# Performance work log

Measured on AMD Instinct MI355X. Metric: run time of the kernel, lower is better.

## Reference

```python
import jax, jax.numpy as jnp
import numpy as np

B, S, I, H, C = 256, 128, 512, 1024, 10
VOCAB = S  # nn.Embedding(seq_length, input_dim)


def _lstm_dir(embeds_tbi, W, b):
    """Run an LSTM over time. embeds_tbi: [S,B,I]; W: [4H, I+H] stacked (g,i,f,o); b: [4H]."""
    h0 = jnp.zeros((B, H), jnp.float32)
    c0 = jnp.zeros((B, H), jnp.float32)

    def step(carry, x_t):
        c, h = carry
        xh = jnp.concatenate([x_t, h], axis=1)          # [B, I+H]
        z = xh @ W.T + b                                 # [B, 4H]
        g, i, f, o = jnp.split(z, 4, axis=1)
        g = jnp.tanh(g)
        i = jax.nn.sigmoid(i)
        f = jax.nn.sigmoid(f)
        o = jax.nn.sigmoid(o)
        new_c = g * i + c * f
        new_h = jnp.tanh(new_c) * o
        return (new_c, new_h), None

    (c_T, h_T), _ = jax.lax.scan(step, (c0, h0), embeds_tbi)
    return h_T


def setup_inputs() -> dict:
    key = jax.random.key(0)
    ks = jax.random.split(key, 8)
    x = jax.random.randint(ks[0], (B, S), 0, VOCAB)
    embed = jax.random.normal(ks[1], (VOCAB, I), jnp.float32) * 0.5
    scale = 1.0 / np.sqrt(I + H)
    fwd_W = jax.random.normal(ks[2], (4 * H, I + H), jnp.float32) * scale  # stacked g,i,f,o
    fwd_b = jax.random.normal(ks[3], (4 * H,), jnp.float32) * 0.02
    bwd_W = jax.random.normal(ks[4], (4 * H, I + H), jnp.float32) * scale
    bwd_b = jax.random.normal(ks[5], (4 * H,), jnp.float32) * 0.02
    p_w = jax.random.normal(ks[6], (C, 2 * H), jnp.float32) * (1.0 / np.sqrt(2 * H))
    p_b = jax.random.normal(ks[7], (C,), jnp.float32) * 0.02
    return {"x": x, "embed": embed, "fwd_W": fwd_W, "fwd_b": fwd_b,
            "bwd_W": bwd_W, "bwd_b": bwd_b, "p_w": p_w, "p_b": p_b}


def reference(x, embed, fwd_W, fwd_b, bwd_W, bwd_b, p_w, p_b):
    embeds = embed[x]                       # [B,S,I]
    emb_t = jnp.transpose(embeds, (1, 0, 2))  # [S,B,I]
    h_fwd = _lstm_dir(emb_t, fwd_W, fwd_b)
    h_bwd = _lstm_dir(emb_t[::-1], bwd_W, bwd_b)
    h_comb = jnp.concatenate([h_fwd, h_bwd], axis=1)  # [B,2H]
    return jax.nn.log_softmax(h_comb @ p_w.T + p_b, axis=1)
```

## Files before the change

### kernel.cpp

```cpp
#include <hip/hip_runtime.h>
#include <hip/hip_bf16.h>
#include <math.h>

#define B 256
#define S 128
#define I_DIM 512
#define H 1024
#define C 10
#define WROW 1536

#define LDS_H 131072

typedef float f32x4 __attribute__((ext_vector_type(4), may_alias));
typedef __bf16 bf16x8 __attribute__((ext_vector_type(8), may_alias));
typedef unsigned int u32x4 __attribute__((ext_vector_type(4), may_alias));
typedef unsigned long long u64;
typedef unsigned long long __attribute__((may_alias)) u64a;

__device__ __forceinline__ unsigned short f2bf(float f) {
    union { float f; unsigned u; } a; a.f = f;
    return (unsigned short)((a.u + 0x7fffu + ((a.u >> 16) & 1u)) >> 16);
}
__device__ __forceinline__ float sigf(float v) { return 1.0f / (1.0f + __expf(-v)); }
__device__ __forceinline__ float tanh_fast(float v) { return 1.0f - 2.0f / (1.0f + __expf(2.0f * v)); }

__global__ void wf_build(const float* __restrict__ fwd_W,
                         const float* __restrict__ bwd_W,
                         __hip_bfloat16* __restrict__ wF) {
    int gid = blockIdx.x * 256 + threadIdx.x;
    int lane = gid & 63, kk = (gid >> 6) & 31, nsub = (gid >> 11) & 255, d = gid >> 19;
    int n_gl = nsub * 16 + (lane & 15);
    int j = n_gl >> 2, g = n_gl & 3;
    int k = kk * 32 + (lane >> 4) * 8;
    const float* W = d ? bwd_W : fwd_W;
    const float* src = W + (size_t)(g * 1024 + j) * WROW + I_DIM + k;
    ushort4 lo = make_ushort4(f2bf(src[0]), f2bf(src[1]), f2bf(src[2]), f2bf(src[3]));
    ushort4 hi = make_ushort4(f2bf(src[4]), f2bf(src[5]), f2bf(src[6]), f2bf(src[7]));
    ushort4* dst = (ushort4*)(wF + (size_t)gid * 8);
    dst[0] = lo; dst[1] = hi;
}

__global__ void projp_kernel(const float* __restrict__ embed,
                             const float* __restrict__ fwd_W,
                             const float* __restrict__ fwd_b,
                             const float* __restrict__ bwd_W,
                             const float* __restrict__ bwd_b,
                             float* __restrict__ projP) {
    __shared__ float wrows[16][520];
    int d  = blockIdx.x >> 8;
    int nc = blockIdx.x & 255;
    int n0 = nc * 16;
    const float* W    = d ? bwd_W : fwd_W;
    const float* bias = d ? bwd_b : fwd_b;
    int tid = threadIdx.x;
    for (int i = tid; i < 16 * 128; i += 256) {
        int r = i >> 7, kc = i & 127;
        *(f32x4*)&wrows[r][kc * 4] = *(const f32x4*)(W + (size_t)(n0 + r) * WROW + kc * 4);
    }
    __syncthreads();
    const int r = tid & 15, vg = tid >> 4;
    const float* eb = embed + (size_t)(vg * 8) * I_DIM;
    f32x4 acc[8] = {};
    for (int kc = 0; kc < 128; kc++) {
        f32x4 w = *(const f32x4*)&wrows[r][kc * 4];
#pragma unroll
        for (int vi = 0; vi < 8; vi++) {
            f32x4 e = *(const f32x4*)(eb + (size_t)vi * I_DIM + kc * 4);
            acc[vi] += w * e;
        }
    }
    const int n = n0 + r, g = n >> 10, j = n & 1023;
    const float bv = bias[n];
    float* outp = projP + ((size_t)d * 1024 + j) * 128 * 4 + g;
#pragma unroll
    for (int vi = 0; vi < 8; vi++) {
        float s = acc[vi][0] + acc[vi][1] + acc[vi][2] + acc[vi][3] + bv;
        outp[(vg * 8 + vi) * 4] = s;
    }
}

__global__ __launch_bounds__(512, 1) void step_kernel(
        const int* __restrict__ x,
        const __hip_bfloat16* __restrict__ wF,
        const float* __restrict__ projP,
        __hip_bfloat16* __restrict__ hbuf,
        float* __restrict__ cws,
        int t) {
    extern __shared__ char smem[];
    const int bid = blockIdx.x;
    const int xcd = bid & 7, idx = bid >> 3;
    const int slot = idx >> 2, bt = idx & 3;
    const int grp = slot * 8 + xcd;
    const int d = grp >> 5, jt = grp & 31;
    const int tid = threadIdx.x, wid = tid >> 6, lane = tid & 63;
    const int l15 = lane & 15, l4 = lane >> 4;
    const int b0 = bt * 64;
    const size_t dBH = (size_t)d * B * H;

    const __hip_bfloat16* wp = wF + (size_t)(d * 256 + jt * 8 + wid) * 16384;

    bf16x8 Ap[8];
    if (t > 0) {
#pragma unroll
        for (int p = 0; p < 8; p++)
            Ap[p] = *(const bf16x8*)(wp + p * 512 + lane * 8);
    }
    const int tt = d ? (S - 1 - t) : t;
    int vv[4];
#pragma unroll
    for (int bs = 0; bs < 4; bs++)
        vv[bs] = x[(b0 + bs * 16 + l15) * S + tt];

    float* cp = cws + ((size_t)bid * 512 + tid) * 4;
    f32x4 cv = {0.f, 0.f, 0.f, 0.f};
    if (t > 0) cv = *(const f32x4*)cp;

    if (t > 0) {
        const __hip_bfloat16* hr = hbuf + (size_t)(t & 1) * 2 * B * H + dBH + (size_t)b0 * H;
#pragma unroll
        for (int i = 0; i < 16; i++) {
            int flat = i * 512 + tid;
            int row = flat >> 7, c16 = flat & 127;
            u32x4 v = *(const u32x4*)(hr + (size_t)row * H + c16 * 8);
            *(u32x4*)(smem + row * 2048 + ((c16 * 16) ^ ((row & 7) << 4))) = v;
        }
    }

    const int j = jt * 32 + wid * 4 + l4;
    const f32x4* pp = (const f32x4*)projP + ((size_t)d * 1024 + j) * 128;
    f32x4 pj[4];
#pragma unroll
    for (int bs = 0; bs < 4; bs++) pj[bs] = pp[vv[bs]];

    f32x4 acc[4] = {};
    if (t > 0) {
        __syncthreads();
        int brow[4], bswz[4];
#pragma unroll
        for (int bs = 0; bs < 4; bs++) {
            int row = bs * 16 + l15;
            brow[bs] = row * 2048;
            bswz[bs] = (row & 7) << 4;
        }
        bf16x8 Bcur[4];
#pragma unroll
        for (int bs = 0; bs < 4; bs++)
            Bcur[bs] = *(const bf16x8*)(smem + brow[bs] + ((l4 * 16) ^ bswz[bs]));
#pragma unroll
        for (int kk = 0; kk < 32; kk++) {
            bf16x8 A = Ap[kk & 7];
            if (kk < 24)
                Ap[kk & 7] = *(const bf16x8*)(wp + (kk + 8) * 512 + lane * 8);
            bf16x8 B0 = Bcur[0], B1 = Bcur[1], B2 = Bcur[2], B3 = Bcur[3];
            if (kk < 31) {
                int koff = (kk + 1) * 64 + l4 * 16;
#pragma unroll
                for (int bs = 0; bs < 4; bs++)
                    Bcur[bs] = *(const bf16x8*)(smem + brow[bs] + (koff ^ bswz[bs]));
            }
            acc[0] = __builtin_amdgcn_mfma_f32_16x16x32_bf16(A, B0, acc[0], 0, 0, 0);
            acc[1] = __builtin_amdgcn_mfma_f32_16x16x32_bf16(A, B1, acc[1], 0, 0, 0);
            acc[2] = __builtin_amdgcn_mfma_f32_16x16x32_bf16(A, B2, acc[2], 0, 0, 0);
            acc[3] = __builtin_amdgcn_mfma_f32_16x16x32_bf16(A, B3, acc[3], 0, 0, 0);
        }
    }

    float hnv[4];
#pragma unroll
    for (int bs = 0; bs < 4; bs++) {
        float zg = acc[bs][0] + pj[bs][0];
        float zi = acc[bs][1] + pj[bs][1];
        float zf = acc[bs][2] + pj[bs][2];
        float zo = acc[bs][3] + pj[bs][3];
        float gg = tanh_fast(zg);
        float ii = sigf(zi);
        float ff = sigf(zf);
        float oo = sigf(zo);
        float cn = gg * ii + cv[bs] * ff;
        cv[bs] = cn;
        hnv[bs] = tanh_fast(cn) * oo;
    }
    *(f32x4*)cp = cv;

    unsigned plo = (unsigned)f2bf(hnv[0]) | ((unsigned)f2bf(hnv[1]) << 16);
    unsigned phi = (unsigned)f2bf(hnv[2]) | ((unsigned)f2bf(hnv[3]) << 16);
    unsigned short o4[4];
#pragma unroll
    for (int p = 0; p < 4; p++) {
        int src = p * 16 + l15;
        unsigned vlo = __shfl(plo, src);
        unsigned vhi = __shfl(phi, src);
        unsigned sel = (l4 < 2) ? vlo : vhi;
        o4[p] = (l4 & 1) ? (unsigned short)(sel >> 16) : (unsigned short)(sel & 0xffffu);
    }
    u64 hv = (u64)o4[0] | ((u64)o4[1] << 16) | ((u64)o4[2] << 32) | ((u64)o4[3] << 48);
    __hip_bfloat16* hw = hbuf + (size_t)((t + 1) & 1) * 2 * B * H + dBH
                         + (size_t)(b0 + lane) * H + jt * 32 + wid * 4;
    *(u64a*)hw = hv;
}

__global__ void head_kernel(const __hip_bfloat16* __restrict__ hbuf,
                            const float* __restrict__ p_w,
                            const float* __restrict__ p_b,
                            float* __restrict__ out) {
    int b = blockIdx.x;
    int lane = threadIdx.x;
    float part[C];
#pragma unroll
    for (int cc = 0; cc < C; cc++) part[cc] = 0.0f;
    for (int jj = lane; jj < 2 * H; jj += 64) {
        float hv = (jj < H)
            ? __bfloat162float(hbuf[(size_t)b * H + jj])
            : __bfloat162float(hbuf[(size_t)B * H + (size_t)b * H + jj - H]);
#pragma unroll
        for (int cc = 0; cc < C; cc++) part[cc] += hv * p_w[cc * 2 * H + jj];
    }
#pragma unroll
    for (int cc = 0; cc < C; cc++) {
        float v = part[cc];
        for (int off = 32; off; off >>= 1) v += __shfl_down(v, off);
        part[cc] = v;
    }
    if (lane == 0) {
        float lg[C];
        float m = -1e30f;
        for (int cc = 0; cc < C; cc++) {
            lg[cc] = part[cc] + p_b[cc];
            m = fmaxf(m, lg[cc]);
        }
        float s = 0.0f;
        for (int cc = 0; cc < C; cc++) s += expf(lg[cc] - m);
        float lse = logf(s) + m;
        for (int cc = 0; cc < C; cc++) out[b * C + cc] = lg[cc] - lse;
    }
}

extern "C" void kernel_launch(void* const* d_in, const int* in_sizes, int n_in,
                              void* d_out, int out_size, void* d_ws, size_t ws_size,
                              hipStream_t stream) {
    const int*   x     = (const int*)d_in[0];
    const float* embed = (const float*)d_in[1];
    const float* fwd_W = (const float*)d_in[2];
    const float* fwd_b = (const float*)d_in[3];
    const float* bwd_W = (const float*)d_in[4];
    const float* bwd_b = (const float*)d_in[5];
    const float* p_w   = (const float*)d_in[6];
    const float* p_b   = (const float*)d_in[7];
    float* outp = (float*)d_out;

    char* ws = (char*)d_ws;
    __hip_bfloat16* wF = (__hip_bfloat16*)ws;  ws += (size_t)2 * 256 * 16384 * 2;
    float* projP = (float*)ws;                 ws += (size_t)2 * 1024 * 128 * 4 * 4;
    __hip_bfloat16* hbuf = (__hip_bfloat16*)ws; ws += (size_t)2 * 2 * B * H * 2;
    float* cws = (float*)ws;                   ws += (size_t)256 * 512 * 4 * 4;

    hipLaunchKernelGGL(wf_build, dim3(4096), dim3(256), 0, stream, fwd_W, bwd_W, wF);
    hipLaunchKernelGGL(projp_kernel, dim3(512), dim3(256), 0, stream,
                       embed, fwd_W, fwd_b, bwd_W, bwd_b, projP);

    hipFuncSetAttribute((const void*)step_kernel,
                        hipFuncAttributeMaxDynamicSharedMemorySize, LDS_H);

    for (int t = 0; t < S; t++)
        hipLaunchKernelGGL(step_kernel, dim3(256), dim3(512), LDS_H, stream,
                           x, wF, projP, hbuf, cws, t);

    hipLaunchKernelGGL(head_kernel, dim3(B), dim3(64), 0, stream,
                       hbuf, p_w, p_b, outp);
}
```

Measured before the change: 1.554 ms.

## Replace per-step launches with a persistent cooperative kernel using flag-based sync

```diff
diff --git a/kernel.cpp b/kernel.cpp
--- a/kernel.cpp
+++ b/kernel.cpp
@@ -15,7 +15,6 @@
 typedef __bf16 bf16x8 __attribute__((ext_vector_type(8), may_alias));
 typedef unsigned int u32x4 __attribute__((ext_vector_type(4), may_alias));
 typedef unsigned long long u64;
-typedef unsigned long long __attribute__((may_alias)) u64a;
 
 __device__ __forceinline__ unsigned short f2bf(float f) {
     union { float f; unsigned u; } a; a.f = f;
@@ -46,7 +45,7 @@
                              const float* __restrict__ bwd_W,
                              const float* __restrict__ bwd_b,
                              float* __restrict__ projP) {
-    __shared__ float wrows[16][520];
+    __shared__ float wrows[16][516];
     int d  = blockIdx.x >> 8;
     int nc = blockIdx.x & 255;
     int n0 = nc * 16;
@@ -79,124 +78,172 @@
     }
 }
 
-__global__ __launch_bounds__(512, 1) void step_kernel(
+__device__ __forceinline__ void stage8(const __hip_bfloat16* hr, int r0, int cc,
+                                       char* smem, int ibase) {
+    const void* p0 = (const void*)(hr + (size_t)((ibase + 0) * 4 + r0) * H + cc * 8);
+    const void* p1 = (const void*)(hr + (size_t)((ibase + 1) * 4 + r0) * H + cc * 8);
+    const void* p2 = (const void*)(hr + (size_t)((ibase + 2) * 4 + r0) * H + cc * 8);
+    const void* p3 = (const void*)(hr + (size_t)((ibase + 3) * 4 + r0) * H + cc * 8);
+    const void* p4 = (const void*)(hr + (size_t)((ibase + 4) * 4 + r0) * H + cc * 8);
+    const void* p5 = (const void*)(hr + (size_t)((ibase + 5) * 4 + r0) * H + cc * 8);
+    const void* p6 = (const void*)(hr + (size_t)((ibase + 6) * 4 + r0) * H + cc * 8);
+    const void* p7 = (const void*)(hr + (size_t)((ibase + 7) * 4 + r0) * H + cc * 8);
+    u32x4 s0, s1, s2, s3, s4, s5, s6, s7;
+    asm volatile(
+        "global_load_dwordx4 %0, %8, off sc0 sc1\n\t"
+        "global_load_dwordx4 %1, %9, off sc0 sc1\n\t"
+        "global_load_dwordx4 %2, %10, off sc0 sc1\n\t"
+        "global_load_dwordx4 %3, %11, off sc0 sc1\n\t"
+        "global_load_dwordx4 %4, %12, off sc0 sc1\n\t"
+        "global_load_dwordx4 %5, %13, off sc0 sc1\n\t"
+        "global_load_dwordx4 %6, %14, off sc0 sc1\n\t"
+        "global_load_dwordx4 %7, %15, off sc0 sc1\n\t"
+        "s_waitcnt vmcnt(0)"
+        : "=&v"(s0), "=&v"(s1), "=&v"(s2), "=&v"(s3),
+          "=&v"(s4), "=&v"(s5), "=&v"(s6), "=&v"(s7)
+        : "v"(p0), "v"(p1), "v"(p2), "v"(p3), "v"(p4), "v"(p5), "v"(p6), "v"(p7)
+        : "memory");
+    int row;
+    row = (ibase + 0) * 4 + r0; *(u32x4*)(smem + row * 2048 + ((cc * 16) ^ ((row & 7) << 4))) = s0;
+    row = (ibase + 1) * 4 + r0; *(u32x4*)(smem + row * 2048 + ((cc * 16) ^ ((row & 7) << 4))) = s1;
+    row = (ibase + 2) * 4 + r0; *(u32x4*)(smem + row * 2048 + ((cc * 16) ^ ((row & 7) << 4))) = s2;
+    row = (ibase + 3) * 4 + r0; *(u32x4*)(smem + row * 2048 + ((cc * 16) ^ ((row & 7) << 4))) = s3;
+    row = (ibase + 4) * 4 + r0; *(u32x4*)(smem + row * 2048 + ((cc * 16) ^ ((row & 7) << 4))) = s4;
+    row = (ibase + 5) * 4 + r0; *(u32x4*)(smem + row * 2048 + ((cc * 16) ^ ((row & 7) << 4))) = s5;
+    row = (ibase + 6) * 4 + r0; *(u32x4*)(smem + row * 2048 + ((cc * 16) ^ ((row & 7) << 4))) = s6;
+    row = (ibase + 7) * 4 + r0; *(u32x4*)(smem + row * 2048 + ((cc * 16) ^ ((row & 7) << 4))) = s7;
+}
+
+__global__ __launch_bounds__(512, 2) void bilstm_persistent(
         const int* __restrict__ x,
         const __hip_bfloat16* __restrict__ wF,
         const float* __restrict__ projP,
         __hip_bfloat16* __restrict__ hbuf,
-        float* __restrict__ cws,
-        int t) {
+        unsigned* __restrict__ flags) {
     extern __shared__ char smem[];
     const int bid = blockIdx.x;
-    const int xcd = bid & 7, idx = bid >> 3;
-    const int slot = idx >> 2, bt = idx & 3;
-    const int grp = slot * 8 + xcd;
-    const int d = grp >> 5, jt = grp & 31;
+    const int xcd = bid & 7;
+    const int d = xcd >> 2, jtHi = xcd & 3;
+    const int idx = bid >> 3;
+    const int jtLo = idx >> 2, bt = idx & 3;
+    const int jt = jtHi * 8 + jtLo;
     const int tid = threadIdx.x, wid = tid >> 6, lane = tid & 63;
     const int l15 = lane & 15, l4 = lane >> 4;
     const int b0 = bt * 64;
     const size_t dBH = (size_t)d * B * H;
 
     const __hip_bfloat16* wp = wF + (size_t)(d * 256 + jt * 8 + wid) * 16384;
-
-    bf16x8 Ap[8];
-    if (t > 0) {
-#pragma unroll
-        for (int p = 0; p < 8; p++)
-            Ap[p] = *(const bf16x8*)(wp + p * 512 + lane * 8);
-    }
-    const int tt = d ? (S - 1 - t) : t;
-    int vv[4];
-#pragma unroll
-    for (int bs = 0; bs < 4; bs++)
-        vv[bs] = x[(b0 + bs * 16 + l15) * S + tt];
-
-    float* cp = cws + ((size_t)bid * 512 + tid) * 4;
-    f32x4 cv = {0.f, 0.f, 0.f, 0.f};
-    if (t > 0) cv = *(const f32x4*)cp;
-
-    if (t > 0) {
-        const __hip_bfloat16* hr = hbuf + (size_t)(t & 1) * 2 * B * H + dBH + (size_t)b0 * H;
-#pragma unroll
-        for (int i = 0; i < 16; i++) {
-            int flat = i * 512 + tid;
-            int row = flat >> 7, c16 = flat & 127;
-            u32x4 v = *(const u32x4*)(hr + (size_t)row * H + c16 * 8);
-            *(u32x4*)(smem + row * 2048 + ((c16 * 16) ^ ((row & 7) << 4))) = v;
-        }
-    }
-
     const int j = jt * 32 + wid * 4 + l4;
     const f32x4* pp = (const f32x4*)projP + ((size_t)d * 1024 + j) * 128;
-    f32x4 pj[4];
-#pragma unroll
-    for (int bs = 0; bs < 4; bs++) pj[bs] = pp[vv[bs]];
-
-    f32x4 acc[4] = {};
-    if (t > 0) {
+    const int r0 = tid >> 7;
+    const int cc = tid & 127;
+
+    int brow[4], bswz[4];
+#pragma unroll
+    for (int bs = 0; bs < 4; bs++) {
+        int row = bs * 16 + l15;
+        brow[bs] = row * 2048;
+        bswz[bs] = (row & 7) << 4;
+    }
+
+    float cst[4] = {0.f, 0.f, 0.f, 0.f};
+
+    for (int t = 0; t < S; t++) {
+        if (t > 0) {
+            if (tid == 0) {
+                const unsigned* p = flags + (size_t)((t - 1) * 8 + d * 4 + bt) * 16;
+                while (__hip_atomic_load(p, __ATOMIC_RELAXED, __HIP_MEMORY_SCOPE_AGENT) < 32u)
+                    __builtin_amdgcn_s_sleep(4);
+            }
+            __syncthreads();
+        }
+
+        bf16x8 Ap[8];
+        if (t > 0) {
+#pragma unroll
+            for (int p = 0; p < 8; p++)
+                Ap[p] = *(const bf16x8*)(wp + p * 512 + lane * 8);
+        }
+        const int tt = d ? (S - 1 - t) : t;
+        int vv[4];
+#pragma unroll
+        for (int bs = 0; bs < 4; bs++)
+            vv[bs] = x[(b0 + bs * 16 + l15) * S + tt];
+
+        if (t > 0) {
+            const __hip_bfloat16* hr = hbuf + (size_t)(t & 1) * 2 * B * H + dBH + (size_t)b0 * H;
+            stage8(hr, r0, cc, smem, 0);
+            stage8(hr, r0, cc, smem, 8);
+        }
+
+        f32x4 pj[4];
+#pragma unroll
+        for (int bs = 0; bs < 4; bs++) pj[bs] = pp[vv[bs]];
+
+        f32x4 acc[4] = {};
+        if (t > 0) {
+            __syncthreads();
+            bf16x8 Bcur[4];
+#pragma unroll
+            for (int bs = 0; bs < 4; bs++)
+                Bcur[bs] = *(const bf16x8*)(smem + brow[bs] + ((l4 * 16) ^ bswz[bs]));
+#pragma unroll
+            for (int kk = 0; kk < 32; kk++) {
+                bf16x8 A = Ap[kk & 7];
+                if (kk < 24)
+                    Ap[kk & 7] = *(const bf16x8*)(wp + (kk + 8) * 512 + lane * 8);
+                bf16x8 B0 = Bcur[0], B1 = Bcur[1], B2 = Bcur[2], B3 = Bcur[3];
+                if (kk < 31) {
+                    int koff = (kk + 1) * 64 + l4 * 16;
+#pragma unroll
+                    for (int bs = 0; bs < 4; bs++)
+                        Bcur[bs] = *(const bf16x8*)(smem + brow[bs] + (koff ^ bswz[bs]));
+                }
+                acc[0] = __builtin_amdgcn_mfma_f32_16x16x32_bf16(A, B0, acc[0], 0, 0, 0);
+                acc[1] = __builtin_amdgcn_mfma_f32_16x16x32_bf16(A, B1, acc[1], 0, 0, 0);
+                acc[2] = __builtin_amdgcn_mfma_f32_16x16x32_bf16(A, B2, acc[2], 0, 0, 0);
+                acc[3] = __builtin_amdgcn_mfma_f32_16x16x32_bf16(A, B3, acc[3], 0, 0, 0);
+            }
+        }
+
+        float hnv[4];
+#pragma unroll
+        for (int bs = 0; bs < 4; bs++) {
+            float zg = acc[bs][0] + pj[bs][0];
+            float zi = acc[bs][1] + pj[bs][1];
+            float zf = acc[bs][2] + pj[bs][2];
+            float zo = acc[bs][3] + pj[bs][3];
+            float gg = tanh_fast(zg);
+            float ii = sigf(zi);
+            float ff = sigf(zf);
+            float oo = sigf(zo);
+            float cn = gg * ii + cst[bs] * ff;
+            cst[bs] = cn;
+            hnv[bs] = tanh_fast(cn) * oo;
+        }
+
+        unsigned plo = (unsigned)f2bf(hnv[0]) | ((unsigned)f2bf(hnv[1]) << 16);
+        unsigned phi = (unsigned)f2bf(hnv[2]) | ((unsigned)f2bf(hnv[3]) << 16);
+        unsigned short o4[4];
+#pragma unroll
+        for (int p = 0; p < 4; p++) {
+            int src = p * 16 + l15;
+            unsigned vlo = __shfl(plo, src);
+            unsigned vhi = __shfl(phi, src);
+            unsigned sel = (l4 < 2) ? vlo : vhi;
+            o4[p] = (l4 & 1) ? (unsigned short)(sel >> 16) : (unsigned short)(sel & 0xffffu);
+        }
+        u64 hv = (u64)o4[0] | ((u64)o4[1] << 16) | ((u64)o4[2] << 32) | ((u64)o4[3] << 48);
+        void* hw = (void*)(hbuf + (size_t)((t + 1) & 1) * 2 * B * H + dBH
+                           + (size_t)(b0 + lane) * H + jt * 32 + wid * 4);
+        asm volatile("global_store_dwordx2 %0, %1, off sc0 sc1"
+                     :: "v"(hw), "v"(hv) : "memory");
+
         __syncthreads();
-        int brow[4], bswz[4];
-#pragma unroll
-        for (int bs = 0; bs < 4; bs++) {
-            int row = bs * 16 + l15;
-            brow[bs] = row * 2048;
-            bswz[bs] = (row & 7) << 4;
-        }
-        bf16x8 Bcur[4];
-#pragma unroll
-        for (int bs = 0; bs < 4; bs++)
-            Bcur[bs] = *(const bf16x8*)(smem + brow[bs] + ((l4 * 16) ^ bswz[bs]));
-#pragma unroll
-        for (int kk = 0; kk < 32; kk++) {
-            bf16x8 A = Ap[kk & 7];
-            if (kk < 24)
-                Ap[kk & 7] = *(const bf16x8*)(wp + (kk + 8) * 512 + lane * 8);
-            bf16x8 B0 = Bcur[0], B1 = Bcur[1], B2 = Bcur[2], B3 = Bcur[3];
-            if (kk < 31) {
-                int koff = (kk + 1) * 64 + l4 * 16;
-#pragma unroll
-                for (int bs = 0; bs < 4; bs++)
-                    Bcur[bs] = *(const bf16x8*)(smem + brow[bs] + (koff ^ bswz[bs]));
-            }
-            acc[0] = __builtin_amdgcn_mfma_f32_16x16x32_bf16(A, B0, acc[0], 0, 0, 0);
-            acc[1] = __builtin_amdgcn_mfma_f32_16x16x32_bf16(A, B1, acc[1], 0, 0, 0);
-            acc[2] = __builtin_amdgcn_mfma_f32_16x16x32_bf16(A, B2, acc[2], 0, 0, 0);
-            acc[3] = __builtin_amdgcn_mfma_f32_16x16x32_bf16(A, B3, acc[3], 0, 0, 0);
-        }
-    }
-
-    float hnv[4];
-#pragma unroll
-    for (int bs = 0; bs < 4; bs++) {
-        float zg = acc[bs][0] + pj[bs][0];
-        float zi = acc[bs][1] + pj[bs][1];
-        float zf = acc[bs][2] + pj[bs][2];
-        float zo = acc[bs][3] + pj[bs][3];
-        float gg = tanh_fast(zg);
-        float ii = sigf(zi);
-        float ff = sigf(zf);
-        float oo = sigf(zo);
-        float cn = gg * ii + cv[bs] * ff;
-        cv[bs] = cn;
-        hnv[bs] = tanh_fast(cn) * oo;
-    }
-    *(f32x4*)cp = cv;
-
-    unsigned plo = (unsigned)f2bf(hnv[0]) | ((unsigned)f2bf(hnv[1]) << 16);
-    unsigned phi = (unsigned)f2bf(hnv[2]) | ((unsigned)f2bf(hnv[3]) << 16);
-    unsigned short o4[4];
-#pragma unroll
-    for (int p = 0; p < 4; p++) {
-        int src = p * 16 + l15;
-        unsigned vlo = __shfl(plo, src);
-        unsigned vhi = __shfl(phi, src);
-        unsigned sel = (l4 < 2) ? vlo : vhi;
-        o4[p] = (l4 & 1) ? (unsigned short)(sel >> 16) : (unsigned short)(sel & 0xffffu);
-    }
-    u64 hv = (u64)o4[0] | ((u64)o4[1] << 16) | ((u64)o4[2] << 32) | ((u64)o4[3] << 48);
-    __hip_bfloat16* hw = hbuf + (size_t)((t + 1) & 1) * 2 * B * H + dBH
-                         + (size_t)(b0 + lane) * H + jt * 32 + wid * 4;
-    *(u64a*)hw = hv;
+        if (tid == 0)
+            __hip_atomic_fetch_add(flags + (size_t)(t * 8 + d * 4 + bt) * 16, 1u,
+                                   __ATOMIC_RELAXED, __HIP_MEMORY_SCOPE_AGENT);
+    }
 }
 
 __global__ void head_kernel(const __hip_bfloat16* __restrict__ hbuf,
@@ -252,18 +299,19 @@
     __hip_bfloat16* wF = (__hip_bfloat16*)ws;  ws += (size_t)2 * 256 * 16384 * 2;
     float* projP = (float*)ws;                 ws += (size_t)2 * 1024 * 128 * 4 * 4;
     __hip_bfloat16* hbuf = (__hip_bfloat16*)ws; ws += (size_t)2 * 2 * B * H * 2;
-    float* cws = (float*)ws;                   ws += (size_t)256 * 512 * 4 * 4;
-
+    unsigned* flags = (unsigned*)ws;           ws += (size_t)S * 8 * 16 * 4;
+
+    hipMemsetAsync(flags, 0, (size_t)S * 8 * 16 * 4, stream);
     hipLaunchKernelGGL(wf_build, dim3(4096), dim3(256), 0, stream, fwd_W, bwd_W, wF);
     hipLaunchKernelGGL(projp_kernel, dim3(512), dim3(256), 0, stream,
                        embed, fwd_W, fwd_b, bwd_W, bwd_b, projP);
 
-    hipFuncSetAttribute((const void*)step_kernel,
+    hipFuncSetAttribute((const void*)bilstm_persistent,
                         hipFuncAttributeMaxDynamicSharedMemorySize, LDS_H);
 
-    for (int t = 0; t < S; t++)
-        hipLaunchKernelGGL(step_kernel, dim3(256), dim3(512), LDS_H, stream,
-                           x, wF, projP, hbuf, cws, t);
+    void* args[] = {(void*)&x, (void*)&wF, (void*)&projP, (void*)&hbuf, (void*)&flags};
+    hipLaunchCooperativeKernel((void*)bilstm_persistent, dim3(256), dim3(512),
+                               args, LDS_H, stream);
 
     hipLaunchKernelGGL(head_kernel, dim3(B), dim3(64), 0, stream,
                        hbuf, p_w, p_b, outp);
```

New measurement: 1.546 ms. About the same (-0.5%).

## Use MFMA for input projection and split h staging into two halves

Applied to the files above, without the earlier changes.

```diff
diff --git a/kernel.cpp b/kernel.cpp
--- a/kernel.cpp
+++ b/kernel.cpp
@@ -20,6 +20,10 @@
 __device__ __forceinline__ unsigned short f2bf(float f) {
     union { float f; unsigned u; } a; a.f = f;
     return (unsigned short)((a.u + 0x7fffu + ((a.u >> 16) & 1u)) >> 16);
+}
+__device__ __forceinline__ float bf2f(unsigned short b) {
+    union { unsigned u; float f; } a; a.u = ((unsigned)b) << 16;
+    return a.f;
 }
 __device__ __forceinline__ float sigf(float v) { return 1.0f / (1.0f + __expf(-v)); }
 __device__ __forceinline__ float tanh_fast(float v) { return 1.0f - 2.0f / (1.0f + __expf(2.0f * v)); }
@@ -40,42 +44,92 @@
     dst[0] = lo; dst[1] = hi;
 }
 
-__global__ void projp_kernel(const float* __restrict__ embed,
-                             const float* __restrict__ fwd_W,
-                             const float* __restrict__ fwd_b,
-                             const float* __restrict__ bwd_W,
-                             const float* __restrict__ bwd_b,
-                             float* __restrict__ projP) {
-    __shared__ float wrows[16][520];
-    int d  = blockIdx.x >> 8;
-    int nc = blockIdx.x & 255;
-    int n0 = nc * 16;
-    const float* W    = d ? bwd_W : fwd_W;
-    const float* bias = d ? bwd_b : fwd_b;
-    int tid = threadIdx.x;
-    for (int i = tid; i < 16 * 128; i += 256) {
-        int r = i >> 7, kc = i & 127;
-        *(f32x4*)&wrows[r][kc * 4] = *(const f32x4*)(W + (size_t)(n0 + r) * WROW + kc * 4);
+__global__ void wxf_build(const float* __restrict__ fwd_W,
+                          const float* __restrict__ bwd_W,
+                          __hip_bfloat16* __restrict__ wxF) {
+    int gid = blockIdx.x * 256 + threadIdx.x;
+    int lane = gid & 63, kk = (gid >> 6) & 15, nsub = (gid >> 10) & 255, d = gid >> 18;
+    int n_gl = nsub * 16 + (lane & 15);
+    int j = n_gl >> 2, g = n_gl & 3;
+    int k = kk * 32 + (lane >> 4) * 8;
+    const float* W = d ? bwd_W : fwd_W;
+    const float* src = W + (size_t)(g * 1024 + j) * WROW + k;
+    ushort4 lo = make_ushort4(f2bf(src[0]), f2bf(src[1]), f2bf(src[2]), f2bf(src[3]));
+    ushort4 hi = make_ushort4(f2bf(src[4]), f2bf(src[5]), f2bf(src[6]), f2bf(src[7]));
+    ushort4* dst = (ushort4*)(wxF + (size_t)gid * 8);
+    dst[0] = lo; dst[1] = hi;
+}
+
+__global__ void ehl_build(const float* __restrict__ embed,
+                          unsigned short* __restrict__ ehl) {
+    int idx = blockIdx.x * 256 + threadIdx.x;
+    float e = embed[idx];
+    unsigned short hb = f2bf(e);
+    unsigned short lb = f2bf(e - bf2f(hb));
+    ehl[idx] = hb;
+    ehl[65536 + idx] = lb;
+}
+
+__global__ __launch_bounds__(256) void projp_mfma(
+        const __hip_bfloat16* __restrict__ wxF,
+        const unsigned short* __restrict__ ehl,
+        const float* __restrict__ fwd_b,
+        const float* __restrict__ bwd_b,
+        float* __restrict__ projP) {
+    extern __shared__ char sm[];
+    const int bid = blockIdx.x;
+    const int d = bid >> 7, jt = (bid >> 2) & 31, vb = bid & 3;
+    const int tid = threadIdx.x, w = tid >> 6, lane = tid & 63;
+    const int l15 = lane & 15, l4 = lane >> 4;
+    const int v0 = vb * 32;
+
+    for (int i = 0; i < 16; i++) {
+        int chunk = i * 256 + tid;
+        int row = chunk >> 6, c16 = chunk & 63;
+        int p = row >> 5, vs = v0 + (row & 31);
+        u32x4 vd = *(const u32x4*)(ehl + ((size_t)p * 128 + vs) * 512 + c16 * 8);
+        *(u32x4*)(sm + row * 1024 + ((c16 * 16) ^ ((row & 7) << 4))) = vd;
     }
     __syncthreads();
-    const int r = tid & 15, vg = tid >> 4;
-    const float* eb = embed + (size_t)(vg * 8) * I_DIM;
-    f32x4 acc[8] = {};
-    for (int kc = 0; kc < 128; kc++) {
-        f32x4 w = *(const f32x4*)&wrows[r][kc * 4];
-#pragma unroll
-        for (int vi = 0; vi < 8; vi++) {
-            f32x4 e = *(const f32x4*)(eb + (size_t)vi * I_DIM + kc * 4);
-            acc[vi] += w * e;
-        }
-    }
-    const int n = n0 + r, g = n >> 10, j = n & 1023;
-    const float bv = bias[n];
-    float* outp = projP + ((size_t)d * 1024 + j) * 128 * 4 + g;
-#pragma unroll
-    for (int vi = 0; vi < 8; vi++) {
-        float s = acc[vi][0] + acc[vi][1] + acc[vi][2] + acc[vi][3] + bv;
-        outp[(vg * 8 + vi) * 4] = s;
+
+    const __hip_bfloat16* ap0 = wxF + ((size_t)((d * 256 + jt * 8 + w * 2 + 0) * 16)) * 512;
+    const __hip_bfloat16* ap1 = wxF + ((size_t)((d * 256 + jt * 8 + w * 2 + 1) * 16)) * 512;
+    int hrow[2], hswz[2], lrow[2], lswz[2];
+#pragma unroll
+    for (int vt = 0; vt < 2; vt++) {
+        int hr = vt * 16 + l15, lr = hr + 32;
+        hrow[vt] = hr * 1024; hswz[vt] = (hr & 7) << 4;
+        lrow[vt] = lr * 1024; lswz[vt] = (lr & 7) << 4;
+    }
+    f32x4 acc[2][2] = {};
+#pragma unroll
+    for (int kk = 0; kk < 16; kk++) {
+        bf16x8 A0 = *(const bf16x8*)(ap0 + kk * 512 + lane * 8);
+        bf16x8 A1 = *(const bf16x8*)(ap1 + kk * 512 + lane * 8);
+        int ko = kk * 64 + l4 * 16;
+        bf16x8 Bh0 = *(const bf16x8*)(sm + hrow[0] + (ko ^ hswz[0]));
+        bf16x8 Bh1 = *(const bf16x8*)(sm + hrow[1] + (ko ^ hswz[1]));
+        bf16x8 Bl0 = *(const bf16x8*)(sm + lrow[0] + (ko ^ lswz[0]));
+        bf16x8 Bl1 = *(const bf16x8*)(sm + lrow[1] + (ko ^ lswz[1]));
+        acc[0][0] = __builtin_amdgcn_mfma_f32_16x16x32_bf16(A0, Bh0, acc[0][0], 0, 0, 0);
+        acc[0][0] = __builtin_amdgcn_mfma_f32_16x16x32_bf16(A0, Bl0, acc[0][0], 0, 0, 0);
+        acc[0][1] = __builtin_amdgcn_mfma_f32_16x16x32_bf16(A0, Bh1, acc[0][1], 0, 0, 0);
+        acc[0][1] = __builtin_amdgcn_mfma_f32_16x16x32_bf16(A0, Bl1, acc[0][1], 0, 0, 0);
+        acc[1][0] = __builtin_amdgcn_mfma_f32_16x16x32_bf16(A1, Bh0, acc[1][0], 0, 0, 0);
+        acc[1][0] = __builtin_amdgcn_mfma_f32_16x16x32_bf16(A1, Bl0, acc[1][0], 0, 0, 0);
+        acc[1][1] = __builtin_amdgcn_mfma_f32_16x16x32_bf16(A1, Bh1, acc[1][1], 0, 0, 0);
+        acc[1][1] = __builtin_amdgcn_mfma_f32_16x16x32_bf16(A1, Bl1, acc[1][1], 0, 0, 0);
+    }
+    const float* bp = d ? bwd_b : fwd_b;
+#pragma unroll
+    for (int nt = 0; nt < 2; nt++) {
+        int j = jt * 32 + w * 8 + nt * 4 + l4;
+        f32x4 bv = { bp[j], bp[1024 + j], bp[2048 + j], bp[3072 + j] };
+#pragma unroll
+        for (int vt = 0; vt < 2; vt++) {
+            int v = v0 + vt * 16 + l15;
+            *(f32x4*)(projP + ((size_t)(d * 1024 + j) * 128 + v) * 4) = acc[nt][vt] + bv;
+        }
     }
 }
 
@@ -88,10 +142,7 @@
         int t) {
     extern __shared__ char smem[];
     const int bid = blockIdx.x;
-    const int xcd = bid & 7, idx = bid >> 3;
-    const int slot = idx >> 2, bt = idx & 3;
-    const int grp = slot * 8 + xcd;
-    const int d = grp >> 5, jt = grp & 31;
+    const int d = bid >> 7, bt = (bid >> 5) & 3, jt = bid & 31;
     const int tid = threadIdx.x, wid = tid >> 6, lane = tid & 63;
     const int l15 = lane & 15, l4 = lane >> 4;
     const int b0 = bt * 64;
@@ -111,30 +162,39 @@
     for (int bs = 0; bs < 4; bs++)
         vv[bs] = x[(b0 + bs * 16 + l15) * S + tt];
 
+    u32x4 sb1[8], sb2[8];
+    int srow[8], sc16[8];
+    if (t > 0) {
+        const __hip_bfloat16* hr = hbuf + (size_t)(t & 1) * 2 * B * H + dBH + (size_t)b0 * H;
+#pragma unroll
+        for (int i = 0; i < 8; i++) {
+            int flat = i * 512 + tid;
+            srow[i] = flat >> 6;
+            sc16[i] = flat & 63;
+            sb1[i] = *(const u32x4*)(hr + (size_t)srow[i] * H + sc16[i] * 8);
+        }
+#pragma unroll
+        for (int i = 0; i < 8; i++)
+            sb2[i] = *(const u32x4*)(hr + (size_t)srow[i] * H + (sc16[i] + 64) * 8);
+    }
+
+    const int j = jt * 32 + wid * 4 + l4;
+    const f32x4* pp = (const f32x4*)projP + ((size_t)d * 1024 + j) * 128;
+    f32x4 pj[4];
+#pragma unroll
+    for (int bs = 0; bs < 4; bs++) pj[bs] = pp[vv[bs]];
+
     float* cp = cws + ((size_t)bid * 512 + tid) * 4;
     f32x4 cv = {0.f, 0.f, 0.f, 0.f};
     if (t > 0) cv = *(const f32x4*)cp;
 
-    if (t > 0) {
-        const __hip_bfloat16* hr = hbuf + (size_t)(t & 1) * 2 * B * H + dBH + (size_t)b0 * H;
-#pragma unroll
-        for (int i = 0; i < 16; i++) {
-            int flat = i * 512 + tid;
-            int row = flat >> 7, c16 = flat & 127;
-            u32x4 v = *(const u32x4*)(hr + (size_t)row * H + c16 * 8);
-            *(u32x4*)(smem + row * 2048 + ((c16 * 16) ^ ((row & 7) << 4))) = v;
-        }
-    }
-
-    const int j = jt * 32 + wid * 4 + l4;
-    const f32x4* pp = (const f32x4*)projP + ((size_t)d * 1024 + j) * 128;
-    f32x4 pj[4];
-#pragma unroll
-    for (int bs = 0; bs < 4; bs++) pj[bs] = pp[vv[bs]];
-
     f32x4 acc[4] = {};
     if (t > 0) {
+#pragma unroll
+        for (int i = 0; i < 8; i++)
+            *(u32x4*)(smem + srow[i] * 2048 + ((sc16[i] * 16) ^ ((srow[i] & 7) << 4))) = sb1[i];
         __syncthreads();
+
         int brow[4], bswz[4];
 #pragma unroll
         for (int bs = 0; bs < 4; bs++) {
@@ -142,22 +202,37 @@
             brow[bs] = row * 2048;
             bswz[bs] = (row & 7) << 4;
         }
-        bf16x8 Bcur[4];
-#pragma unroll
-        for (int bs = 0; bs < 4; bs++)
-            Bcur[bs] = *(const bf16x8*)(smem + brow[bs] + ((l4 * 16) ^ bswz[bs]));
-#pragma unroll
-        for (int kk = 0; kk < 32; kk++) {
+
+#pragma unroll
+        for (int kk = 0; kk < 16; kk++) {
+            bf16x8 A = Ap[kk & 7];
+            Ap[kk & 7] = *(const bf16x8*)(wp + (kk + 8) * 512 + lane * 8);
+            int koff = kk * 64 + l4 * 16;
+            bf16x8 B0 = *(const bf16x8*)(smem + brow[0] + (koff ^ bswz[0]));
+            bf16x8 B1 = *(const bf16x8*)(smem + brow[1] + (koff ^ bswz[1]));
+            bf16x8 B2 = *(const bf16x8*)(smem + brow[2] + (koff ^ bswz[2]));
+            bf16x8 B3 = *(const bf16x8*)(smem + brow[3] + (koff ^ bswz[3]));
+            acc[0] = __builtin_amdgcn_mfma_f32_16x16x32_bf16(A, B0, acc[0], 0, 0, 0);
+            acc[1] = __builtin_amdgcn_mfma_f32_16x16x32_bf16(A, B1, acc[1], 0, 0, 0);
+            acc[2] = __builtin_amdgcn_mfma_f32_16x16x32_bf16(A, B2, acc[2], 0, 0, 0);
+            acc[3] = __builtin_amdgcn_mfma_f32_16x16x32_bf16(A, B3, acc[3], 0, 0, 0);
+        }
+
+#pragma unroll
+        for (int i = 0; i < 8; i++)
+            *(u32x4*)(smem + srow[i] * 2048 + (((sc16[i] + 64) * 16) ^ ((srow[i] & 7) << 4))) = sb2[i];
+        __syncthreads();
+
+#pragma unroll
+        for (int kk = 16; kk < 32; kk++) {
             bf16x8 A = Ap[kk & 7];
             if (kk < 24)
                 Ap[kk & 7] = *(const bf16x8*)(wp + (kk + 8) * 512 + lane * 8);
-            bf16x8 B0 = Bcur[0], B1 = Bcur[1], B2 = Bcur[2], B3 = Bcur[3];
-            if (kk < 31) {
-                int koff = (kk + 1) * 64 + l4 * 16;
-#pragma unroll
-                for (int bs = 0; bs < 4; bs++)
-                    Bcur[bs] = *(const bf16x8*)(smem + brow[bs] + (koff ^ bswz[bs]));
-            }
+            int koff = kk * 64 + l4 * 16;
+            bf16x8 B0 = *(const bf16x8*)(smem + brow[0] + (koff ^ bswz[0]));
+            bf16x8 B1 = *(const bf16x8*)(smem + brow[1] + (koff ^ bswz[1]));
+            bf16x8 B2 = *(const bf16x8*)(smem + brow[2] + (koff ^ bswz[2]));
+            bf16x8 B3 = *(const bf16x8*)(smem + brow[3] + (koff ^ bswz[3]));
             acc[0] = __builtin_amdgcn_mfma_f32_16x16x32_bf16(A, B0, acc[0], 0, 0, 0);
             acc[1] = __builtin_amdgcn_mfma_f32_16x16x32_bf16(A, B1, acc[1], 0, 0, 0);
             acc[2] = __builtin_amdgcn_mfma_f32_16x16x32_bf16(A, B2, acc[2], 0, 0, 0);
@@ -249,18 +324,24 @@
     float* outp = (float*)d_out;
 
     char* ws = (char*)d_ws;
-    __hip_bfloat16* wF = (__hip_bfloat16*)ws;  ws += (size_t)2 * 256 * 16384 * 2;
-    float* projP = (float*)ws;                 ws += (size_t)2 * 1024 * 128 * 4 * 4;
+    __hip_bfloat16* wF  = (__hip_bfloat16*)ws;  ws += (size_t)2 * 256 * 16384 * 2;
+    __hip_bfloat16* wxF = (__hip_bfloat16*)ws;
+    float* cws = (float*)ws;                    ws += (size_t)2 * 256 * 8192 * 2;
+    unsigned short* ehl = (unsigned short*)ws;  ws += (size_t)2 * 128 * 512 * 2;
+    float* projP = (float*)ws;                  ws += (size_t)2 * 1024 * 128 * 4 * 4;
     __hip_bfloat16* hbuf = (__hip_bfloat16*)ws; ws += (size_t)2 * 2 * B * H * 2;
-    float* cws = (float*)ws;                   ws += (size_t)256 * 512 * 4 * 4;
 
     hipLaunchKernelGGL(wf_build, dim3(4096), dim3(256), 0, stream, fwd_W, bwd_W, wF);
-    hipLaunchKernelGGL(projp_kernel, dim3(512), dim3(256), 0, stream,
-                       embed, fwd_W, fwd_b, bwd_W, bwd_b, projP);
+    hipLaunchKernelGGL(wxf_build, dim3(2048), dim3(256), 0, stream, fwd_W, bwd_W, wxF);
+    hipLaunchKernelGGL(ehl_build, dim3(256), dim3(256), 0, stream, embed, ehl);
+
+    hipFuncSetAttribute((const void*)projp_mfma,
+                        hipFuncAttributeMaxDynamicSharedMemorySize, 65536);
+    hipLaunchKernelGGL(projp_mfma, dim3(256), dim3(256), 65536, stream,
+                       wxF, ehl, fwd_b, bwd_b, projP);
 
     hipFuncSetAttribute((const void*)step_kernel,
                         hipFuncAttributeMaxDynamicSharedMemorySize, LDS_H);
-
     for (int t = 0; t < S; t++)
         hipLaunchKernelGGL(step_kernel, dim3(256), dim3(512), LDS_H, stream,
                            x, wF, projP, hbuf, cws, t);
```

Measured after the change: 1.648 ms. +6.0%, slower.
